# Performance work log

Measured on AMD Instinct MI355X. Metric: run time of the kernel, lower is better.

## Reference

```python
import jax, jax.numpy as jnp
import numpy as np

B, N_SERIES, T, HIDDEN = 256, 512, 512, 1024
EPS = 1e-5  # BatchNorm1d default eps


def setup_inputs() -> dict:
    key = jax.random.key(0)
    ks = jax.random.split(key, 6)
    s_in = 1.0 / np.sqrt(N_SERIES)
    s_hid = 1.0 / np.sqrt(2 * HIDDEN)
    s_out = 1.0 / np.sqrt(HIDDEN)
    return {
        "x": jax.random.normal(ks[0], (B, N_SERIES, T), dtype=jnp.float32),
        # input_layer: Linear(n_series -> hidden)
        "Wi": jax.random.uniform(ks[1], (HIDDEN, N_SERIES), jnp.float32, -s_in, s_in),
        "bi": jnp.zeros((HIDDEN,), jnp.float32),
        # hidden_layer: Linear(2*hidden -> hidden)
        "Wh": jax.random.uniform(ks[2], (HIDDEN, 2 * HIDDEN), jnp.float32, -s_hid, s_hid),
        "bh": jnp.zeros((HIDDEN,), jnp.float32),
        # BatchNorm1d(hidden) affine params
        "gamma": jnp.ones((HIDDEN,), jnp.float32),
        "beta": jnp.zeros((HIDDEN,), jnp.float32),
        # last_layer: Linear(hidden -> n_series)
        "Wl": jax.random.uniform(ks[3], (N_SERIES, HIDDEN), jnp.float32, -s_out, s_out),
        "bl": jnp.zeros((N_SERIES,), jnp.float32),
    }


def reference(x, Wi, bi, Wh, bh, gamma, beta, Wl, bl):
    # x: [B, n_series, T] -> time-major [T, B, n_series]
    xt = jnp.transpose(x, (2, 0, 1))
    h0 = jnp.zeros((x.shape[0], Wh.shape[0]), x.dtype)

    def step(h, x_t):
        inp = x_t @ Wi.T + bi                              # [B, H]
        emb = jnp.concatenate([inp, h], axis=1)            # [B, 2H]
        h_new = jnp.tanh(emb @ Wh.T + bh)                  # [B, H]
        return h_new, None

    hidden, _ = jax.lax.scan(step, h0, xt)
    # BatchNorm1d, training-mode batch statistics (biased variance)
    mean = jnp.mean(hidden, axis=0)
    var = jnp.var(hidden, axis=0)
    h_bn = gamma * (hidden - mean) / jnp.sqrt(var + EPS) + beta
    return h_bn @ Wl.T + bl                                # [B, n_series]
```

## Files before the change

### kernel.cpp

```cpp
#include <hip/hip_runtime.h>

typedef _Float16 f16;
typedef _Float16 half8 __attribute__((ext_vector_type(8)));
typedef float f32x4 __attribute__((ext_vector_type(4)));

#define HIDDEN 1024
#define NSER 512
#define BATCH 256
#define TSTEPS 512

__device__ __forceinline__ float tanh_fast(float x) {
  x = fminf(15.0f, fmaxf(-15.0f, x));
  float e = __expf(2.0f * x);
  return (e - 1.0f) / (e + 1.0f);
}


__global__ __launch_bounds__(256) void convert_whl_kernel(const float* __restrict__ Wh,
                                                          f16* __restrict__ WhLh) {
  int idx = blockIdx.x * 256 + threadIdx.x;
  int j = idx >> 10, k = idx & 1023;
  WhLh[idx] = (f16)Wh[((size_t)j << 11) + k];
}

__global__ __launch_bounds__(256) void convert_wl_kernel(const float* __restrict__ Wl,
                                                         f16* __restrict__ Wlh) {
  int idx = blockIdx.x * 256 + threadIdx.x;
  Wlh[idx] = (f16)Wl[idx];
}

__global__ __launch_bounds__(256) void transpose_wi_kernel(const float* __restrict__ Wi,
                                                           f16* __restrict__ WiT) {
  __shared__ float tile[32][33];
  int tx = threadIdx.x & 31, ty = threadIdx.x >> 5;
  int c0 = blockIdx.x * 32;
  int r0 = blockIdx.y * 32;
#pragma unroll
  for (int i = 0; i < 32; i += 8)
    tile[ty + i][tx] = Wi[(size_t)(r0 + ty + i) * NSER + c0 + tx];
  __syncthreads();
#pragma unroll
  for (int i = 0; i < 32; i += 8)
    WiT[(size_t)(c0 + ty + i) * HIDDEN + r0 + tx] = (f16)tile[tx][ty + i];
}

__global__ __launch_bounds__(256) void transpose_x_kernel(const float* __restrict__ x,
                                                          f16* __restrict__ xT) {
  __shared__ float tile[32][33];
  int b = blockIdx.z;
  int t0 = blockIdx.x * 32, n0 = blockIdx.y * 32;
  int tx = threadIdx.x & 31, ty = threadIdx.x >> 5;
#pragma unroll
  for (int i = 0; i < 32; i += 8)
    tile[ty + i][tx] = x[((size_t)b * NSER + n0 + ty + i) * TSTEPS + t0 + tx];
  __syncthreads();
#pragma unroll
  for (int i = 0; i < 32; i += 8)
    xT[((size_t)(t0 + ty + i) * BATCH + b) * NSER + n0 + tx] = (f16)tile[tx][ty + i];
}

__global__ __launch_bounds__(256) void beff_kernel(const float* __restrict__ Wh,
                                                   const float* __restrict__ bi,
                                                   const float* __restrict__ bh,
                                                   float* __restrict__ beff) {
  __shared__ float red[256];
  int j = blockIdx.x;
  float s = 0.f;
  for (int k = threadIdx.x; k < HIDDEN; k += 256)
    s += Wh[(size_t)j * 2048 + k] * bi[k];
  red[threadIdx.x] = s;
  __syncthreads();
  for (int off = 128; off > 0; off >>= 1) {
    if (threadIdx.x < (unsigned)off) red[threadIdx.x] += red[threadIdx.x + off];
    __syncthreads();
  }
  if (threadIdx.x == 0) beff[j] = bh[j] + red[0];
}

template <bool OUT_F16, bool HAS_BIAS>
__global__ __launch_bounds__(256) void gemm_f16_kernel(const f16* __restrict__ A,
                                                       const f16* __restrict__ B,
                                                       const float* __restrict__ bias,
                                                       void* __restrict__ Cp,
                                                       int M, int N, int K) {
  (void)M;
  __shared__ f16 As[128 * 64];
  __shared__ f16 Bs[128 * 64];
  const int tid = threadIdx.x;
  const int l = tid & 63, w = tid >> 6;
  const int wr = w >> 1, wc = w & 1;
  const int lr = l & 15, lg = l >> 4;
  const size_t m0 = (size_t)blockIdx.y * 128, n0 = (size_t)blockIdx.x * 128;
  f32x4 acc[4][4] = {};
  for (int k0 = 0; k0 < K; k0 += 64) {
    half8 ar[4], br[4];
#pragma unroll
    for (int c = 0; c < 4; ++c) {
      int Gq = c * 256 + tid;
      int row = Gq >> 3, colg = Gq & 7;
      ar[c] = *(const half8*)&A[(m0 + row) * K + k0 + colg * 8];
      br[c] = *(const half8*)&B[(n0 + row) * K + k0 + colg * 8];
    }
    __syncthreads();
#pragma unroll
    for (int c = 0; c < 4; ++c) {
      int Gq = c * 256 + tid;
      *(half8*)&As[Gq * 8] = ar[c];
      *(half8*)&Bs[Gq * 8] = br[c];
    }
    __syncthreads();
#pragma unroll
    for (int ks = 0; ks < 2; ++ks) {
      half8 a[4], b[4];
#pragma unroll
      for (int i = 0; i < 4; ++i)
        a[i] = *(const half8*)&As[(wr * 64 + i * 16 + lr) * 64 + ks * 32 + lg * 8];
#pragma unroll
      for (int i = 0; i < 4; ++i)
        b[i] = *(const half8*)&Bs[(wc * 64 + i * 16 + lr) * 64 + ks * 32 + lg * 8];
#pragma unroll
      for (int mi = 0; mi < 4; ++mi)
#pragma unroll
        for (int ni = 0; ni < 4; ++ni)
          acc[mi][ni] = __builtin_amdgcn_mfma_f32_16x16x32_f16(a[mi], b[ni], acc[mi][ni], 0, 0, 0);
    }
  }
#pragma unroll
  for (int mi = 0; mi < 4; ++mi) {
#pragma unroll
    for (int ni = 0; ni < 4; ++ni) {
      size_t n = n0 + wc * 64 + ni * 16 + lr;
      float bv = 0.f;
      if constexpr (HAS_BIAS) bv = bias[n];
#pragma unroll
      for (int r = 0; r < 4; ++r) {
        size_t m = m0 + wr * 64 + mi * 16 + lg * 4 + r;
        float v = acc[mi][ni][r] + bv;
        if constexpr (OUT_F16)
          ((f16*)Cp)[m * (size_t)N + n] = (f16)v;
        else
          ((float*)Cp)[m * (size_t)N + n] = v;
      }
    }
  }
}

__global__ __launch_bounds__(256) void rnn_kernel(const float* __restrict__ Wh,
                                                  const f16* __restrict__ Z,
                                                  f16* hb0, f16* hb1,
                                                  float* __restrict__ h_final,
                                                  unsigned int* cnt) {
  const int bid = blockIdx.x;
  const int g = bid >> 4, q = bid & 15;
  const int tid = threadIdx.x;
  const int l = tid & 63, w = tid >> 6;
  const int lr = l & 15, lg = l >> 4;
  const int b0 = g * 16;
  const int jcol = q * 64 + w * 16 + lr;

  half8 breg[32];
#pragma unroll
  for (int ks = 0; ks < 32; ++ks) {
    const float* s = &Wh[(size_t)jcol * 2048 + HIDDEN + ks * 32 + lg * 8];
    half8 hv;
#pragma unroll
    for (int i = 0; i < 8; ++i) hv[i] = (f16)s[i];
    breg[ks] = hv;
  }

  __shared__ f16 hs[16 * HIDDEN];

  for (int t = 0; t < TSTEPS; ++t) {
    const f16* hprev = (t & 1) ? hb1 : hb0;
    f16* hnext = (t & 1) ? hb0 : hb1;

    const f16* zp = &Z[((size_t)t * BATCH + b0 + lg * 4) * HIDDEN + jcol];
    f16 z0 = zp[0], z1 = zp[HIDDEN], z2 = zp[2 * HIDDEN], z3 = zp[3 * HIDDEN];

    half8 hv[8];
    if (t == 0) {
#pragma unroll
      for (int i = 0; i < 8; ++i) {
        int G = i * 256 + tid;
        int row = G >> 7, gI = G & 127;
        hv[i] = *(const half8*)&hprev[(size_t)(b0 + row) * HIDDEN + gI * 8];
      }
    } else {
#pragma unroll
      for (int i = 0; i < 8; ++i) {
        int G = i * 256 + tid;
        int row = G >> 7, gI = G & 127;
        const f16* src = &hprev[(size_t)(b0 + row) * HIDDEN + gI * 8];
        asm volatile("global_load_dwordx4 %0, %1, off sc0 sc1"
                     : "=v"(hv[i])
                     : "v"(src));
      }
    }
    asm volatile("s_waitcnt vmcnt(0)" ::: "memory");

#pragma unroll
    for (int i = 0; i < 8; ++i) {
      int G = i * 256 + tid;
      int row = G >> 7, gI = G & 127;
      *(half8*)&hs[row * HIDDEN + ((gI ^ (row & 7)) * 8)] = hv[i];
    }
    __syncthreads();

    f32x4 acc = {0.f, 0.f, 0.f, 0.f};
#pragma unroll
    for (int ks = 0; ks < 32; ++ks) {
      int gA = ks * 4 + lg;
      half8 a = *(const half8*)&hs[lr * HIDDEN + ((gA ^ (lr & 7)) * 8)];
      acc = __builtin_amdgcn_mfma_f32_16x16x32_f16(a, breg[ks], acc, 0, 0, 0);
    }

    float v0 = tanh_fast(acc[0] + (float)z0);
    float v1 = tanh_fast(acc[1] + (float)z1);
    float v2 = tanh_fast(acc[2] + (float)z2);
    float v3 = tanh_fast(acc[3] + (float)z3);

    if (t == TSTEPS - 1) {
      h_final[(size_t)(b0 + lg * 4 + 0) * HIDDEN + jcol] = v0;
      h_final[(size_t)(b0 + lg * 4 + 1) * HIDDEN + jcol] = v1;
      h_final[(size_t)(b0 + lg * 4 + 2) * HIDDEN + jcol] = v2;
      h_final[(size_t)(b0 + lg * 4 + 3) * HIDDEN + jcol] = v3;
    } else {
      unsigned s0 = (unsigned)__builtin_bit_cast(unsigned short, (f16)v0);
      unsigned s1 = (unsigned)__builtin_bit_cast(unsigned short, (f16)v1);
      unsigned s2 = (unsigned)__builtin_bit_cast(unsigned short, (f16)v2);
      unsigned s3 = (unsigned)__builtin_bit_cast(unsigned short, (f16)v3);
      f16* p0 = &hnext[(size_t)(b0 + lg * 4 + 0) * HIDDEN + jcol];
      asm volatile("global_store_short %0, %1, off sc0 sc1" ::"v"(p0), "v"(s0) : "memory");
      asm volatile("global_store_short %0, %1, off sc0 sc1" ::"v"(p0 + HIDDEN), "v"(s1) : "memory");
      asm volatile("global_store_short %0, %1, off sc0 sc1" ::"v"(p0 + 2 * HIDDEN), "v"(s2) : "memory");
      asm volatile("global_store_short %0, %1, off sc0 sc1" ::"v"(p0 + 3 * HIDDEN), "v"(s3) : "memory");
      asm volatile("s_waitcnt vmcnt(0)" ::: "memory");
      __syncthreads();
      if (tid == 0)
        __hip_atomic_fetch_add(&cnt[g * TSTEPS + t], 1u, __ATOMIC_RELAXED,
                               __HIP_MEMORY_SCOPE_AGENT);
      int guard = 0;
      while (__hip_atomic_load(&cnt[g * TSTEPS + t], __ATOMIC_RELAXED,
                               __HIP_MEMORY_SCOPE_AGENT) < 16u) {
        if (++guard > (1 << 20)) break;
      }
      asm volatile("" ::: "memory");
    }
  }
}

__global__ __launch_bounds__(256) void bn_kernel(const float* __restrict__ hf,
                                                 const float* __restrict__ gamma,
                                                 const float* __restrict__ beta,
                                                 f16* __restrict__ hbn) {
  int j = blockIdx.x * 256 + threadIdx.x;
  float s1 = 0.f, s2 = 0.f;
  for (int b = 0; b < BATCH; ++b) {
    float v = hf[(size_t)b * HIDDEN + j];
    s1 += v;
    s2 += v * v;
  }
  float mean = s1 * (1.f / BATCH);
  float var = s2 * (1.f / BATCH) - mean * mean;
  float sc = gamma[j] * rsqrtf(var + 1e-5f);
  float sh = beta[j] - mean * sc;
  for (int b = 0; b < BATCH; ++b)
    hbn[(size_t)b * HIDDEN + j] = (f16)(hf[(size_t)b * HIDDEN + j] * sc + sh);
}

extern "C" void kernel_launch(void* const* d_in, const int* in_sizes, int n_in,
                              void* d_out, int out_size, void* d_ws, size_t ws_size,
                              hipStream_t stream) {
  (void)in_sizes; (void)n_in; (void)out_size;
  const float* x     = (const float*)d_in[0];
  const float* Wi    = (const float*)d_in[1];
  const float* bi    = (const float*)d_in[2];
  const float* Wh    = (const float*)d_in[3];
  const float* bh    = (const float*)d_in[4];
  const float* gamma = (const float*)d_in[5];
  const float* beta  = (const float*)d_in[6];
  const float* Wl    = (const float*)d_in[7];
  const float* bl    = (const float*)d_in[8];
  float* out = (float*)d_out;

  char* wsp = (char*)d_ws;
  size_t off = 0;
  auto alloc = [&](size_t bytes) -> void* {
    void* p = (void*)(wsp + off);
    off += (bytes + 255) & ~(size_t)255;
    return p;
  };
  f16*      Zb    = (f16*)alloc((size_t)TSTEPS * BATCH * HIDDEN * 2);
  f16*      xT    = (f16*)alloc((size_t)TSTEPS * BATCH * NSER * 2);
  f16*      WhLh  = (f16*)alloc((size_t)HIDDEN * HIDDEN * 2);
  f16*      WiT   = (f16*)alloc((size_t)NSER * HIDDEN * 2);
  f16*      Wlh   = (f16*)alloc((size_t)NSER * HIDDEN * 2);
  f16*      Weff  = (f16*)alloc((size_t)HIDDEN * NSER * 2);
  float*    beff  = (float*)alloc(HIDDEN * 4);
  f16*      hbuf0 = (f16*)alloc((size_t)BATCH * HIDDEN * 2);
  f16*      hbuf1 = (f16*)alloc((size_t)BATCH * HIDDEN * 2);
  float*    hfin  = (float*)alloc((size_t)BATCH * HIDDEN * 4);
  f16*      hbn   = (f16*)alloc((size_t)BATCH * HIDDEN * 2);
  unsigned* cnt   = (unsigned*)alloc(16 * TSTEPS * 4);
  if (off > ws_size) return;

  hipMemsetAsync(cnt, 0, 16 * TSTEPS * 4, stream);
  hipMemsetAsync(hbuf0, 0, (size_t)BATCH * HIDDEN * 2, stream);

  convert_whl_kernel<<<4096, 256, 0, stream>>>(Wh, WhLh);
  transpose_wi_kernel<<<dim3(16, 32), 256, 0, stream>>>(Wi, WiT);
  convert_wl_kernel<<<2048, 256, 0, stream>>>(Wl, Wlh);
  beff_kernel<<<1024, 256, 0, stream>>>(Wh, bi, bh, beff);
  gemm_f16_kernel<true, false><<<dim3(4, 8), 256, 0, stream>>>(WhLh, WiT, nullptr, Weff,
                                                               1024, NSER, HIDDEN);
  transpose_x_kernel<<<dim3(16, 16, 256), 256, 0, stream>>>(x, xT);
  gemm_f16_kernel<true, true><<<dim3(8, 1024), 256, 0, stream>>>(xT, Weff, beff, Zb,
                                                                 TSTEPS * BATCH, HIDDEN, NSER);
  rnn_kernel<<<256, 256, 0, stream>>>(Wh, Zb, hbuf0, hbuf1, hfin, cnt);
  bn_kernel<<<4, 256, 0, stream>>>(hfin, gamma, beta, hbn);
  gemm_f16_kernel<false, true><<<dim3(4, 2), 256, 0, stream>>>(hbn, Wlh, bl, out,
                                                               BATCH, NSER, HIDDEN);
}
```

Baseline: 2.504 ms.

## Replace atomic-counter barrier with per-block step flags and use 512-thread RNN blocks

```diff
diff --git a/kernel.cpp b/kernel.cpp
--- a/kernel.cpp
+++ b/kernel.cpp
@@ -145,18 +145,18 @@
   }
 }
 
-__global__ __launch_bounds__(256) void rnn_kernel(const float* __restrict__ Wh,
+__global__ __launch_bounds__(512) void rnn_kernel(const float* __restrict__ Wh,
                                                   const f16* __restrict__ Z,
                                                   f16* hb0, f16* hb1,
                                                   float* __restrict__ h_final,
-                                                  unsigned int* cnt) {
+                                                  unsigned int* canary) {
   const int bid = blockIdx.x;
-  const int g = bid >> 4, q = bid & 15;
+  const int g = bid >> 3, q = bid & 7;
   const int tid = threadIdx.x;
   const int l = tid & 63, w = tid >> 6;
   const int lr = l & 15, lg = l >> 4;
   const int b0 = g * 16;
-  const int jcol = q * 64 + w * 16 + lr;
+  const int jcol = q * 128 + w * 16 + lr;
 
   half8 breg[32];
 #pragma unroll
@@ -177,42 +177,50 @@
     const f16* zp = &Z[((size_t)t * BATCH + b0 + lg * 4) * HIDDEN + jcol];
     f16 z0 = zp[0], z1 = zp[HIDDEN], z2 = zp[2 * HIDDEN], z3 = zp[3 * HIDDEN];
 
-    half8 hv[8];
-    if (t == 0) {
-#pragma unroll
-      for (int i = 0; i < 8; ++i) {
-        int G = i * 256 + tid;
-        int row = G >> 7, gI = G & 127;
-        hv[i] = *(const half8*)&hprev[(size_t)(b0 + row) * HIDDEN + gI * 8];
-      }
-    } else {
-#pragma unroll
-      for (int i = 0; i < 8; ++i) {
-        int G = i * 256 + tid;
-        int row = G >> 7, gI = G & 127;
-        const f16* src = &hprev[(size_t)(b0 + row) * HIDDEN + gI * 8];
-        asm volatile("global_load_dwordx4 %0, %1, off sc0 sc1"
-                     : "=v"(hv[i])
-                     : "v"(src));
-      }
+    {
+      const unsigned* cp = &canary[g * 8 + (l & 7)];
+      unsigned cv;
+      int guard = 0;
+      do {
+        asm volatile("global_load_dword %0, %1, off sc0 sc1\n\ts_waitcnt vmcnt(0)"
+                     : "=v"(cv)
+                     : "v"(cp)
+                     : "memory");
+      } while (__ballot(cv < (unsigned)t) != 0ull && ++guard < (1 << 20));
+    }
+
+    half8 hv[4];
+#pragma unroll
+    for (int i = 0; i < 4; ++i) {
+      int G = i * 512 + tid;
+      int row = G >> 7, gI = G & 127;
+      const f16* src = &hprev[(size_t)(b0 + row) * HIDDEN + gI * 8];
+      asm volatile("global_load_dwordx4 %0, %1, off sc0 sc1" : "=v"(hv[i]) : "v"(src));
     }
     asm volatile("s_waitcnt vmcnt(0)" ::: "memory");
 
 #pragma unroll
-    for (int i = 0; i < 8; ++i) {
-      int G = i * 256 + tid;
+    for (int i = 0; i < 4; ++i) {
+      int G = i * 512 + tid;
       int row = G >> 7, gI = G & 127;
       *(half8*)&hs[row * HIDDEN + ((gI ^ (row & 7)) * 8)] = hv[i];
     }
     __syncthreads();
 
-    f32x4 acc = {0.f, 0.f, 0.f, 0.f};
-#pragma unroll
-    for (int ks = 0; ks < 32; ++ks) {
-      int gA = ks * 4 + lg;
-      half8 a = *(const half8*)&hs[lr * HIDDEN + ((gA ^ (lr & 7)) * 8)];
-      acc = __builtin_amdgcn_mfma_f32_16x16x32_f16(a, breg[ks], acc, 0, 0, 0);
-    }
+    f32x4 acc0 = {0.f, 0.f, 0.f, 0.f}, acc1 = acc0, acc2 = acc0, acc3 = acc0;
+#pragma unroll
+    for (int ks = 0; ks < 32; ks += 4) {
+      int gA0 = ks * 4 + lg;
+      half8 a0 = *(const half8*)&hs[lr * HIDDEN + ((gA0 ^ (lr & 7)) * 8)];
+      half8 a1 = *(const half8*)&hs[lr * HIDDEN + (((gA0 + 4) ^ (lr & 7)) * 8)];
+      half8 a2 = *(const half8*)&hs[lr * HIDDEN + (((gA0 + 8) ^ (lr & 7)) * 8)];
+      half8 a3 = *(const half8*)&hs[lr * HIDDEN + (((gA0 + 12) ^ (lr & 7)) * 8)];
+      acc0 = __builtin_amdgcn_mfma_f32_16x16x32_f16(a0, breg[ks + 0], acc0, 0, 0, 0);
+      acc1 = __builtin_amdgcn_mfma_f32_16x16x32_f16(a1, breg[ks + 1], acc1, 0, 0, 0);
+      acc2 = __builtin_amdgcn_mfma_f32_16x16x32_f16(a2, breg[ks + 2], acc2, 0, 0, 0);
+      acc3 = __builtin_amdgcn_mfma_f32_16x16x32_f16(a3, breg[ks + 3], acc3, 0, 0, 0);
+    }
+    f32x4 acc = (acc0 + acc1) + (acc2 + acc3);
 
     float v0 = tanh_fast(acc[0] + (float)z0);
     float v1 = tanh_fast(acc[1] + (float)z1);
@@ -236,15 +244,12 @@
       asm volatile("global_store_short %0, %1, off sc0 sc1" ::"v"(p0 + 3 * HIDDEN), "v"(s3) : "memory");
       asm volatile("s_waitcnt vmcnt(0)" ::: "memory");
       __syncthreads();
-      if (tid == 0)
-        __hip_atomic_fetch_add(&cnt[g * TSTEPS + t], 1u, __ATOMIC_RELAXED,
-                               __HIP_MEMORY_SCOPE_AGENT);
-      int guard = 0;
-      while (__hip_atomic_load(&cnt[g * TSTEPS + t], __ATOMIC_RELAXED,
-                               __HIP_MEMORY_SCOPE_AGENT) < 16u) {
-        if (++guard > (1 << 20)) break;
+      if (tid == 0) {
+        unsigned nv = (unsigned)(t + 1);
+        asm volatile("global_store_dword %0, %1, off sc0 sc1" ::"v"(&canary[g * 8 + q]),
+                     "v"(nv)
+                     : "memory");
       }
-      asm volatile("" ::: "memory");
     }
   }
 }
@@ -301,10 +306,10 @@
   f16*      hbuf1 = (f16*)alloc((size_t)BATCH * HIDDEN * 2);
   float*    hfin  = (float*)alloc((size_t)BATCH * HIDDEN * 4);
   f16*      hbn   = (f16*)alloc((size_t)BATCH * HIDDEN * 2);
-  unsigned* cnt   = (unsigned*)alloc(16 * TSTEPS * 4);
+  unsigned* canary = (unsigned*)alloc(16 * 8 * 4);
   if (off > ws_size) return;
 
-  hipMemsetAsync(cnt, 0, 16 * TSTEPS * 4, stream);
+  hipMemsetAsync(canary, 0, 16 * 8 * 4, stream);
   hipMemsetAsync(hbuf0, 0, (size_t)BATCH * HIDDEN * 2, stream);
 
   convert_whl_kernel<<<4096, 256, 0, stream>>>(Wh, WhLh);
@@ -316,7 +321,7 @@
   transpose_x_kernel<<<dim3(16, 16, 256), 256, 0, stream>>>(x, xT);
   gemm_f16_kernel<true, true><<<dim3(8, 1024), 256, 0, stream>>>(xT, Weff, beff, Zb,
                                                                  TSTEPS * BATCH, HIDDEN, NSER);
-  rnn_kernel<<<256, 256, 0, stream>>>(Wh, Zb, hbuf0, hbuf1, hfin, cnt);
+  rnn_kernel<<<128, 512, 0, stream>>>(Wh, Zb, hbuf0, hbuf1, hfin, canary);
   bn_kernel<<<4, 256, 0, stream>>>(hfin, gamma, beta, hbn);
   gemm_f16_kernel<false, true><<<dim3(4, 2), 256, 0, stream>>>(hbn, Wlh, bl, out,
                                                                BATCH, NSER, HIDDEN);
```

Result: slower. 2.794 ms (+11.6%).
